# Kernel optimization log

Measured on AMD Instinct MI355X. Metric: run time of the kernel, lower is better.

## Reference

```python
import jax, jax.numpy as jnp
import numpy as np

B, S, H = 2, 2048, 1024
NH, HD = 16, 64
SCALE = HD ** -0.5


def setup_inputs() -> dict:
    key = jax.random.key(0)
    k1, k2, k3, k4 = jax.random.split(key, 4)
    hidden_states = jax.random.normal(k1, (B, S, H), dtype=jnp.float32)
    attention_mask = jax.random.randint(k2, (B, S), 0, 2, dtype=jnp.int32)
    # xavier-uniform-ish init scale
    w_qkv = jax.random.normal(k3, (3 * H, H), dtype=jnp.float32) * (2.0 / (H + 3 * H)) ** 0.5
    w_out = jax.random.normal(k4, (H, H), dtype=jnp.float32) * (1.0 / H) ** 0.5
    return {"hidden_states": hidden_states, "attention_mask": attention_mask,
            "w_qkv": w_qkv, "w_out": w_out}


def reference(hidden_states, attention_mask, w_qkv, w_out):
    b, s, _ = hidden_states.shape
    qkv = hidden_states @ w_qkv.T                      # [B,S,3H]
    q, k, v = jnp.split(qkv, 3, axis=-1)
    # [B,S,H] -> [B,NH,S,HD]
    reshape = lambda x: x.reshape(b, s, NH, HD).transpose(0, 2, 1, 3)
    q, k, v = reshape(q), reshape(k), reshape(v)
    scores = jnp.einsum('bhqd,bhkd->bhqk', q, k) * SCALE   # [B,NH,S,S]
    mask = attention_mask[:, None, None, :] == 0           # [B,1,1,S]
    scores = jnp.where(mask, -jnp.inf, scores)
    attn = jax.nn.softmax(scores, axis=-1)                 # dropout p: eval mode -> identity
    out = jnp.einsum('bhqk,bhkd->bhqd', attn, v)           # [B,NH,S,HD]
    out = out.transpose(0, 2, 1, 3).reshape(b, s, H)
    return out @ w_out.T
```

## Files before the change

kernel.cpp:

```cpp
#include <hip/hip_runtime.h>
#include <string.h>


typedef __bf16    bf16x8 __attribute__((ext_vector_type(8)));
typedef _Float16  f16x4  __attribute__((ext_vector_type(4)));
typedef _Float16  f16x2  __attribute__((ext_vector_type(2)));
typedef float     f32x4  __attribute__((ext_vector_type(4)));

#define NTOK   4096
#define HDIM   1024
#define SEQ    2048
#define NHEAD  16
#define F2SHIFT 4.0f
#define QSCALE  0.18033688f
#define LSTRIDE 68

__device__ __forceinline__ float bf2f(unsigned short u) {
    union { unsigned int i; float f; } x;
    x.i = ((unsigned int)u) << 16;
    return x.f;
}
__device__ __forceinline__ unsigned short f2bf(float f) {
    union { __bf16 h; unsigned short u; } x;
    x.h = (__bf16)f;
    return x.u;
}
__device__ __forceinline__ unsigned short f2h(float f) {
    union { _Float16 h; unsigned short u; } x;
    x.h = (_Float16)f;
    return x.u;
}
__device__ __forceinline__ f16x2 pkrtz(float a, float b) {
    union { __fp16 __attribute__((ext_vector_type(2))) i; f16x2 o; } x;
    x.i = __builtin_amdgcn_cvt_pkrtz(a, b);
    return x.o;
}

__device__ __forceinline__ int detect_f32(const unsigned short* hs) {
    unsigned int idx = (threadIdx.x & 63) * 4096u;
    float f = bf2f(hs[idx]);
    return __any(!(fabsf(f) < 1e4f));
}

typedef const __attribute__((address_space(1))) unsigned int* gptr_u32;
typedef __attribute__((address_space(3))) unsigned int* lptr_u32;

__device__ __forceinline__ void async16(const unsigned short* g, unsigned short* l) {
    __builtin_amdgcn_global_load_lds((gptr_u32)g, (lptr_u32)l, 16, 0, 0);
}

__global__ void convert3_kernel(const void* __restrict__ s0, const void* __restrict__ s1,
                                const void* __restrict__ s2, unsigned short* __restrict__ dst) {
    const int isf32 = detect_f32((const unsigned short*)s0);
    if (!isf32) return;
    int g = blockIdx.x * blockDim.x + threadIdx.x;
    const int stride = gridDim.x * blockDim.x;
    for (; g < 1048576; g += stride) {
        int i = g * 8;
        const void* src; int off;
        if (i < 4194304)      { src = s0; off = i; }
        else if (i < 7340032) { src = s1; off = i - 4194304; }
        else                  { src = s2; off = i - 7340032; }
        const float* s = (const float*)src + off;
        unsigned short o[8];
#pragma unroll
        for (int j = 0; j < 8; j++) o[j] = f2bf(s[j]);
        *(uint4*)(dst + i) = *(const uint4*)o;
    }
}

__global__ __launch_bounds__(256) void gemm_qkv(
    const unsigned short* __restrict__ Xc, const unsigned short* __restrict__ Wc,
    const unsigned short* __restrict__ Xraw, const unsigned short* __restrict__ Wraw,
    unsigned short* __restrict__ q_out, unsigned short* __restrict__ k_out,
    unsigned short* __restrict__ v_out) {
    const int K = 1024;
    __shared__ __align__(16) unsigned short Xs0[128 * 32];
    __shared__ __align__(16) unsigned short Xs1[128 * 32];
    __shared__ __align__(16) unsigned short Ws0[128 * 32];
    __shared__ __align__(16) unsigned short Ws1[128 * 32];

    const int isf32 = detect_f32(Xraw);
    const unsigned short* X = isf32 ? Xc : Xraw;
    const unsigned short* W = isf32 ? Wc : Wraw;

    const int t = threadIdx.x;
    const int w = t >> 6, lane = t & 63, quad = lane >> 4, lr = lane & 15;
    const int wrow = (w >> 1) * 64, wcol = (w & 1) * 64;

    const int hid = blockIdx.x;
    const int xcd = hid & 7, r = hid >> 3;
    const int by = xcd * 4 + r / 24;
    const int bx = r % 24;
    const int m0 = by * 128, n0 = bx * 128;
    const bool vblk = (n0 >= 2048);

    f32x4 acc[4][4];
#pragma unroll
    for (int mi = 0; mi < 4; mi++)
#pragma unroll
        for (int ni = 0; ni < 4; ni++) acc[mi][ni] = (f32x4){0.f, 0.f, 0.f, 0.f};

    const int srow = w * 32 + (lane >> 2);
    const int scol = (lane & 3) * 8;
    const unsigned short* xg = X + (size_t)(m0 + srow) * K + scol;
    const unsigned short* wg = W + (size_t)(n0 + srow) * K + scol;
    unsigned short* xl0 = &Xs0[w * 1024];
    unsigned short* xl1 = &Xs1[w * 1024];
    unsigned short* wl0 = &Ws0[w * 1024];
    unsigned short* wl1 = &Ws1[w * 1024];

    for (int k0 = 0; k0 < K; k0 += 64) {
        __syncthreads();
        async16(xg + k0, xl0);
        async16(xg + k0 + 16 * K, xl0 + 512);
        async16(xg + k0 + 32, xl1);
        async16(xg + k0 + 32 + 16 * K, xl1 + 512);
        async16(wg + k0, wl0);
        async16(wg + k0 + 16 * K, wl0 + 512);
        async16(wg + k0 + 32, wl1);
        async16(wg + k0 + 32 + 16 * K, wl1 + 512);
        __syncthreads();
#pragma unroll
        for (int h = 0; h < 2; h++) {
            const unsigned short* Xh = h ? Xs1 : Xs0;
            const unsigned short* Wh = h ? Ws1 : Ws0;
            bf16x8 af[4], bfr[4];
#pragma unroll
            for (int mi = 0; mi < 4; mi++)
                af[mi] = *(const bf16x8*)&Xh[(wrow + mi * 16 + lr) * 32 + quad * 8];
#pragma unroll
            for (int ni = 0; ni < 4; ni++)
                bfr[ni] = *(const bf16x8*)&Wh[(wcol + ni * 16 + lr) * 32 + quad * 8];
            if (!vblk) {
#pragma unroll
                for (int mi = 0; mi < 4; mi++)
#pragma unroll
                    for (int ni = 0; ni < 4; ni++)
                        acc[mi][ni] = __builtin_amdgcn_mfma_f32_16x16x32_bf16(af[mi], bfr[ni], acc[mi][ni], 0, 0, 0);
            } else {
#pragma unroll
                for (int mi = 0; mi < 4; mi++)
#pragma unroll
                    for (int ni = 0; ni < 4; ni++)
                        acc[mi][ni] = __builtin_amdgcn_mfma_f32_16x16x32_bf16(bfr[ni], af[mi], acc[mi][ni], 0, 0, 0);
            }
        }
    }

    if (!vblk) {
#pragma unroll
        for (int mi = 0; mi < 4; mi++)
#pragma unroll
            for (int ni = 0; ni < 4; ni++)
#pragma unroll
                for (int rr = 0; rr < 4; rr++) {
                    int mrow = m0 + wrow + mi * 16 + quad * 4 + rr;
                    int j = n0 + wcol + ni * 16 + lr;
                    float val = acc[mi][ni][rr];
                    int which = j >> 10, rem = j & 1023;
                    int nh = rem >> 6, hd = rem & 63;
                    int b = mrow >> 11, s = mrow & 2047;
                    size_t dst = ((size_t)(b * NHEAD + nh) * SEQ + s) * 64 + hd;
                    if (which == 0) q_out[dst] = f2bf(val * QSCALE);
                    else            k_out[dst] = f2bf(val);
                }
    } else {
#pragma unroll
        for (int mi = 0; mi < 4; mi++)
#pragma unroll
            for (int ni = 0; ni < 4; ni++)
#pragma unroll
                for (int rr = 0; rr < 4; rr++) {
                    int n = n0 + wcol + ni * 16 + quad * 4 + rr;
                    int m = m0 + wrow + mi * 16 + lr;
                    float val = acc[mi][ni][rr];
                    int rem = n & 1023;
                    int nh = rem >> 6, hd = rem & 63;
                    int b = m >> 11, s = m & 2047;
                    size_t dst = ((size_t)(b * NHEAD + nh) * 64 + hd) * SEQ + s;
                    v_out[dst] = f2h(val);
                }
    }
}

__global__ __launch_bounds__(256) void gemm_out(
    const unsigned short* __restrict__ X, const unsigned short* __restrict__ Wc,
    const unsigned short* __restrict__ Wraw,
    void* __restrict__ d_out, const unsigned short* __restrict__ hs_raw) {
    const int K = 1024, N = 1024;
    __shared__ __align__(16) unsigned short Xs0[64 * 32];
    __shared__ __align__(16) unsigned short Xs1[64 * 32];
    __shared__ __align__(16) unsigned short Xs2[64 * 32];
    __shared__ __align__(16) unsigned short Xs3[64 * 32];
    __shared__ __align__(16) unsigned short Ws0[128 * 32];
    __shared__ __align__(16) unsigned short Ws1[128 * 32];
    __shared__ __align__(16) unsigned short Ws2[128 * 32];
    __shared__ __align__(16) unsigned short Ws3[128 * 32];

    const int isf32 = detect_f32(hs_raw);
    const unsigned short* W = isf32 ? Wc : Wraw;

    const int t = threadIdx.x;
    const int w = t >> 6, lane = t & 63, quad = lane >> 4, lr = lane & 15;
    const int wrow = (w >> 1) * 32, wcol = (w & 1) * 64;
    const int m0 = blockIdx.y * 64, n0 = blockIdx.x * 128;

    f32x4 acc[2][4];
#pragma unroll
    for (int mi = 0; mi < 2; mi++)
#pragma unroll
        for (int ni = 0; ni < 4; ni++) acc[mi][ni] = (f32x4){0.f, 0.f, 0.f, 0.f};

    const int sxrow = w * 16 + (lane >> 2);
    const int swrow = w * 32 + (lane >> 2);
    const int scol = (lane & 3) * 8;
    const unsigned short* xg = X + (size_t)(m0 + sxrow) * K + scol;
    const unsigned short* wg = W + (size_t)(n0 + swrow) * K + scol;
    unsigned short* xl[4] = { &Xs0[w * 512], &Xs1[w * 512], &Xs2[w * 512], &Xs3[w * 512] };
    unsigned short* wl[4] = { &Ws0[w * 1024], &Ws1[w * 1024], &Ws2[w * 1024], &Ws3[w * 1024] };

    for (int k0 = 0; k0 < K; k0 += 128) {
        __syncthreads();
#pragma unroll
        for (int j = 0; j < 4; j++) {
            async16(xg + k0 + j * 32, xl[j]);
            async16(wg + k0 + j * 32, wl[j]);
            async16(wg + k0 + j * 32 + 16 * K, wl[j] + 512);
        }
        __syncthreads();
#pragma unroll
        for (int h = 0; h < 4; h++) {
            const unsigned short* Xh = (h == 0) ? Xs0 : (h == 1) ? Xs1 : (h == 2) ? Xs2 : Xs3;
            const unsigned short* Wh = (h == 0) ? Ws0 : (h == 1) ? Ws1 : (h == 2) ? Ws2 : Ws3;
            bf16x8 af[2], bfr[4];
#pragma unroll
            for (int mi = 0; mi < 2; mi++)
                af[mi] = *(const bf16x8*)&Xh[(wrow + mi * 16 + lr) * 32 + quad * 8];
#pragma unroll
            for (int ni = 0; ni < 4; ni++)
                bfr[ni] = *(const bf16x8*)&Wh[(wcol + ni * 16 + lr) * 32 + quad * 8];
#pragma unroll
            for (int mi = 0; mi < 2; mi++)
#pragma unroll
                for (int ni = 0; ni < 4; ni++)
                    acc[mi][ni] = __builtin_amdgcn_mfma_f32_16x16x32_bf16(af[mi], bfr[ni], acc[mi][ni], 0, 0, 0);
        }
    }

#pragma unroll
    for (int mi = 0; mi < 2; mi++)
#pragma unroll
        for (int ni = 0; ni < 4; ni++)
#pragma unroll
            for (int rr = 0; rr < 4; rr++) {
                int mrow = m0 + wrow + mi * 16 + quad * 4 + rr;
                int j = n0 + wcol + ni * 16 + lr;
                float val = acc[mi][ni][rr];
                size_t dst = (size_t)mrow * N + j;
                if (isf32) ((float*)d_out)[dst] = val;
                else ((unsigned short*)d_out)[dst] = f2bf(val);
            }
}

__global__ __launch_bounds__(256, 2) void flash_attn_v12(
    const unsigned short* __restrict__ q, const unsigned short* __restrict__ k,
    const unsigned short* __restrict__ vt, const int* __restrict__ mask,
    unsigned short* __restrict__ attn_out) {
    __shared__ __align__(16) unsigned short Ks[128 * LSTRIDE];
    __shared__ __align__(16) unsigned short Vt0[64 * LSTRIDE];
    __shared__ __align__(16) unsigned short Vt1[64 * LSTRIDE];
    __shared__ __align__(16) float Msk[136];

    const int t = threadIdx.x;
    const int w = t >> 6, lane = t & 63, quad = lane >> 4, lr = lane & 15;
    const int bh = blockIdx.x, b = bh >> 4, h = bh & 15;
    const int q0 = blockIdx.y * 128;

    const unsigned short* qb = q + (size_t)bh * SEQ * 64;
    const unsigned short* kb = k + (size_t)bh * SEQ * 64;
    const unsigned short* vtb = vt + (size_t)bh * 64 * SEQ;
    const int* mb = mask + b * SEQ;

    bf16x8 qf[2][2];
#pragma unroll
    for (int qg = 0; qg < 2; qg++) {
        const unsigned short* qrow = qb + (size_t)(q0 + w * 32 + qg * 16 + lr) * 64 + quad * 8;
        qf[qg][0] = *(const bf16x8*)qrow;
        qf[qg][1] = *(const bf16x8*)(qrow + 32);
    }

    f32x4 oacc[2][4];
#pragma unroll
    for (int qg = 0; qg < 2; qg++)
#pragma unroll
        for (int dt = 0; dt < 4; dt++) oacc[qg][dt] = (f32x4){0.f, 0.f, 0.f, 0.f};
    float l_st[2] = {0.f, 0.f};

    const int sr = t >> 2;
    const int sc = (t & 3) * 16;

    for (int kk0 = 0; kk0 < SEQ; kk0 += 128) {
        const uint4* kp0 = (const uint4*)(kb + (size_t)(kk0 + sr) * 64 + sc);
        const uint4* kp1 = (const uint4*)(kb + (size_t)(kk0 + 64 + sr) * 64 + sc);
        const uint4* vp0 = (const uint4*)(vtb + (size_t)sr * SEQ + kk0 + sc);
        const uint4* vp1 = (const uint4*)(vtb + (size_t)sr * SEQ + kk0 + 64 + sc);
        uint4 k0a = kp0[0], k0b = kp0[1];
        uint4 k1a = kp1[0], k1b = kp1[1];
        uint4 v0a = vp0[0], v0b = vp0[1];
        uint4 v1a = vp1[0], v1b = vp1[1];
        float mval = 0.f;
        if (t < 128) mval = (mb[kk0 + t] == 0) ? -1e30f : -F2SHIFT;

        __syncthreads();
        *(uint4*)&Ks[sr * LSTRIDE + sc] = k0a;
        *(uint4*)&Ks[sr * LSTRIDE + sc + 8] = k0b;
        *(uint4*)&Ks[(64 + sr) * LSTRIDE + sc] = k1a;
        *(uint4*)&Ks[(64 + sr) * LSTRIDE + sc + 8] = k1b;
        *(uint4*)&Vt0[sr * LSTRIDE + sc] = v0a;
        *(uint4*)&Vt0[sr * LSTRIDE + sc + 8] = v0b;
        *(uint4*)&Vt1[sr * LSTRIDE + sc] = v1a;
        *(uint4*)&Vt1[sr * LSTRIDE + sc + 8] = v1b;
        if (t < 128) Msk[t] = mval;
        __syncthreads();

        __builtin_amdgcn_s_setprio(1);
#pragma unroll
        for (int mt = 0; mt < 8; mt++) {
            bf16x8 a1h0 = *(bf16x8*)&Ks[(mt * 16 + lr) * LSTRIDE + quad * 8];
            bf16x8 a1h1 = *(bf16x8*)&Ks[(mt * 16 + lr) * LSTRIDE + 32 + quad * 8];
            const unsigned short* vb_ = (mt < 4) ? Vt0 : Vt1;
            const int mcol = (mt & 3) * 16;
            f16x4 a2[4];
#pragma unroll
            for (int dt = 0; dt < 4; dt++)
                a2[dt] = *(const f16x4*)&vb_[(dt * 16 + lr) * LSTRIDE + mcol + quad * 4];
            float4 mv = *(const float4*)&Msk[mt * 16 + quad * 4];
            f32x4 zi = (f32x4){mv.x, mv.y, mv.z, mv.w};

#pragma unroll
            for (int qg = 0; qg < 2; qg++) {
                f32x4 z = __builtin_amdgcn_mfma_f32_16x16x32_bf16(a1h0, qf[qg][0], zi, 0, 0, 0);
                z = __builtin_amdgcn_mfma_f32_16x16x32_bf16(a1h1, qf[qg][1], z, 0, 0, 0);
                float p0 = __builtin_amdgcn_exp2f(z[0]);
                float p1 = __builtin_amdgcn_exp2f(z[1]);
                float p2 = __builtin_amdgcn_exp2f(z[2]);
                float p3 = __builtin_amdgcn_exp2f(z[3]);
                l_st[qg] += (p0 + p1) + (p2 + p3);
                f16x2 ab = pkrtz(p0, p1);
                f16x2 cd = pkrtz(p2, p3);
                f16x4 b2;
                b2[0] = ab[0]; b2[1] = ab[1]; b2[2] = cd[0]; b2[3] = cd[1];
#pragma unroll
                for (int dt = 0; dt < 4; dt++)
                    oacc[qg][dt] = __builtin_amdgcn_mfma_f32_16x16x16f16(a2[dt], b2, oacc[qg][dt], 0, 0, 0);
            }
        }
        __builtin_amdgcn_s_setprio(0);
    }

    float inv[2];
#pragma unroll
    for (int qg = 0; qg < 2; qg++) {
        float s = l_st[qg];
        s += __shfl_xor(s, 16);
        s += __shfl_xor(s, 32);
        inv[qg] = 1.0f / s;
    }
#pragma unroll
    for (int qg = 0; qg < 2; qg++) {
        size_t tok = (size_t)(b * SEQ + q0 + w * 32 + qg * 16 + lr);
#pragma unroll
        for (int dt = 0; dt < 4; dt++)
#pragma unroll
            for (int rr = 0; rr < 4; rr++)
                attn_out[tok * HDIM + h * 64 + dt * 16 + quad * 4 + rr] =
                    f2bf(oacc[qg][dt][rr] * inv[qg]);
    }
}

extern "C" void kernel_launch(void* const* d_in, const int* in_sizes, int n_in,
                              void* d_out, int out_size, void* d_ws, size_t ws_size,
                              hipStream_t stream) {
    const void* hs_raw = d_in[0];
    const int* mask = (const int*)d_in[1];
    const void* wqkv_raw = d_in[2];
    const void* wout_raw = d_in[3];

    char* wsb = (char*)d_ws;
    unsigned short* hs_c = (unsigned short*)(wsb + 256);
    unsigned short* wqkv_c = hs_c + 4194304;
    unsigned short* wout_c = wqkv_c + 3145728;
    unsigned short* qw = wout_c + 1048576;
    unsigned short* kw = qw + 4194304;
    unsigned short* vtw = kw + 4194304;
    unsigned short* ao = vtw + 4194304;

    convert3_kernel<<<1024, 256, 0, stream>>>(hs_raw, wqkv_raw, wout_raw, hs_c);

    gemm_qkv<<<768, 256, 0, stream>>>(hs_c, wqkv_c,
                                      (const unsigned short*)hs_raw,
                                      (const unsigned short*)wqkv_raw,
                                      qw, kw, vtw);
    flash_attn_v12<<<dim3(32, 16), 256, 0, stream>>>(qw, kw, vtw, mask, ao);
    gemm_out<<<dim3(8, 64), 256, 0, stream>>>(ao, wout_c,
                                              (const unsigned short*)wout_raw, d_out,
                                              (const unsigned short*)hs_raw);
}
```

Baseline: 187.1 us.

## Split flash attention over two sequential key-range launches with partial merge

Runs the attention kernel twice, each pass covering half of the key/value sequence. The first pass stores unnormalized fp16 partial outputs and row sums in reused workspace. The second pass adds those partials and normalizes. Because the grid size is unchanged, this mostly shortens each pass rather than adding concurrency. It costs an extra launch, extra global traffic for the partials, and a precision or overflow risk from keeping unnormalized sums in fp16.

Result: slower. 195.4 us (+4.4%).

```diff
diff --git a/kernel.cpp b/kernel.cpp
--- a/kernel.cpp
+++ b/kernel.cpp
@@ -14,6 +14,7 @@
 #define F2SHIFT 4.0f
 #define QSCALE  0.18033688f
 #define LSTRIDE 68
+#define KHALF  1024
 
 __device__ __forceinline__ float bf2f(unsigned short u) {
     union { unsigned int i; float f; } x;
@@ -29,6 +30,11 @@
     union { _Float16 h; unsigned short u; } x;
     x.h = (_Float16)f;
     return x.u;
+}
+__device__ __forceinline__ float h2f(unsigned short u) {
+    union { unsigned short u; _Float16 h; } x;
+    x.u = u;
+    return (float)x.h;
 }
 __device__ __forceinline__ f16x2 pkrtz(float a, float b) {
     union { __fp16 __attribute__((ext_vector_type(2))) i; f16x2 o; } x;
@@ -263,10 +269,12 @@
             }
 }
 
-__global__ __launch_bounds__(256, 2) void flash_attn_v12(
+__global__ __launch_bounds__(256, 2) void flash_attn_v13(
     const unsigned short* __restrict__ q, const unsigned short* __restrict__ k,
     const unsigned short* __restrict__ vt, const int* __restrict__ mask,
-    unsigned short* __restrict__ attn_out) {
+    unsigned short* __restrict__ attn_out,
+    unsigned short* __restrict__ opart, float* __restrict__ lpart,
+    const int kbase) {
     __shared__ __align__(16) unsigned short Ks[128 * LSTRIDE];
     __shared__ __align__(16) unsigned short Vt0[64 * LSTRIDE];
     __shared__ __align__(16) unsigned short Vt1[64 * LSTRIDE];
@@ -300,7 +308,7 @@
     const int sr = t >> 2;
     const int sc = (t & 3) * 16;
 
-    for (int kk0 = 0; kk0 < SEQ; kk0 += 128) {
+    for (int kk0 = kbase; kk0 < kbase + KHALF; kk0 += 128) {
         const uint4* kp0 = (const uint4*)(kb + (size_t)(kk0 + sr) * 64 + sc);
         const uint4* kp1 = (const uint4*)(kb + (size_t)(kk0 + 64 + sr) * 64 + sc);
         const uint4* vp0 = (const uint4*)(vtb + (size_t)sr * SEQ + kk0 + sc);
@@ -359,23 +367,43 @@
         __builtin_amdgcn_s_setprio(0);
     }
 
-    float inv[2];
+    float lsum[2];
 #pragma unroll
     for (int qg = 0; qg < 2; qg++) {
         float s = l_st[qg];
         s += __shfl_xor(s, 16);
         s += __shfl_xor(s, 32);
-        inv[qg] = 1.0f / s;
-    }
-#pragma unroll
-    for (int qg = 0; qg < 2; qg++) {
-        size_t tok = (size_t)(b * SEQ + q0 + w * 32 + qg * 16 + lr);
-#pragma unroll
-        for (int dt = 0; dt < 4; dt++)
-#pragma unroll
-            for (int rr = 0; rr < 4; rr++)
-                attn_out[tok * HDIM + h * 64 + dt * 16 + quad * 4 + rr] =
-                    f2bf(oacc[qg][dt][rr] * inv[qg]);
+        lsum[qg] = s;
+    }
+
+    if (kbase == 0) {
+#pragma unroll
+        for (int qg = 0; qg < 2; qg++) {
+            const int qrow = q0 + w * 32 + qg * 16 + lr;
+            if (quad == 0) lpart[bh * 2048 + qrow] = lsum[qg];
+            size_t tok = (size_t)(b * SEQ + qrow);
+#pragma unroll
+            for (int dt = 0; dt < 4; dt++)
+#pragma unroll
+                for (int rr = 0; rr < 4; rr++)
+                    opart[tok * HDIM + h * 64 + dt * 16 + quad * 4 + rr] =
+                        f2h(oacc[qg][dt][rr]);
+        }
+    } else {
+#pragma unroll
+        for (int qg = 0; qg < 2; qg++) {
+            const int qrow = q0 + w * 32 + qg * 16 + lr;
+            const float inv = 1.0f / (lsum[qg] + lpart[bh * 2048 + qrow]);
+            size_t tok = (size_t)(b * SEQ + qrow);
+#pragma unroll
+            for (int dt = 0; dt < 4; dt++) {
+                const unsigned short* op = &opart[tok * HDIM + h * 64 + dt * 16 + quad * 4];
+#pragma unroll
+                for (int rr = 0; rr < 4; rr++)
+                    attn_out[tok * HDIM + h * 64 + dt * 16 + quad * 4 + rr] =
+                        f2bf((oacc[qg][dt][rr] + h2f(op[rr])) * inv);
+            }
+        }
     }
 }
 
@@ -396,13 +424,17 @@
     unsigned short* vtw = kw + 4194304;
     unsigned short* ao = vtw + 4194304;
 
+    unsigned short* opart = hs_c;
+    float* lpart = (float*)wqkv_c;
+
     convert3_kernel<<<1024, 256, 0, stream>>>(hs_raw, wqkv_raw, wout_raw, hs_c);
 
     gemm_qkv<<<768, 256, 0, stream>>>(hs_c, wqkv_c,
                                       (const unsigned short*)hs_raw,
                                       (const unsigned short*)wqkv_raw,
                                       qw, kw, vtw);
-    flash_attn_v12<<<dim3(32, 16), 256, 0, stream>>>(qw, kw, vtw, mask, ao);
+    flash_attn_v13<<<dim3(32, 16), 256, 0, stream>>>(qw, kw, vtw, mask, ao, opart, lpart, 0);
+    flash_attn_v13<<<dim3(32, 16), 256, 0, stream>>>(qw, kw, vtw, mask, ao, opart, lpart, 1024);
     gemm_out<<<dim3(8, 64), 256, 0, stream>>>(ao, wout_c,
                                               (const unsigned short*)wout_raw, d_out,
                                               (const unsigned short*)hs_raw);
```
